# Performance work log

Measured on AMD Instinct MI355X. Metric: run time of the kernel, lower is better.

Reference implementation:

```python
import jax, jax.numpy as jnp
import numpy as np

SEQ, BATCH, IN_DIM, HID, LAYERS = 1024, 256, 64, 128, 2


def setup_inputs() -> dict:
    key = jax.random.key(0)
    ks = jax.random.split(key, 9)
    s = 1.0 / np.sqrt(HID)  # torch nn.RNN init: U(-1/sqrt(H), 1/sqrt(H))
    u = lambda k, shape: jax.random.uniform(k, shape, jnp.float32, -s, s)
    return {
        "x": jax.random.normal(ks[0], (SEQ, BATCH, IN_DIM), jnp.float32),
        "W_ih0": u(ks[1], (HID, IN_DIM)),
        "b_ih0": u(ks[2], (HID,)),
        "W_hh0": u(ks[3], (HID, HID)),
        "b_hh0": u(ks[4], (HID,)),
        "W_ih1": u(ks[5], (HID, HID)),
        "b_ih1": u(ks[6], (HID,)),
        "W_hh1": u(ks[7], (HID, HID)),
        "b_hh1": u(ks[8], (HID,)),
    }


def _rnn_layer(x, W_ih, b_ih, W_hh, b_hh):
    # x: (S, B, F). Precompute the input projection once (big GEMM),
    # keeping only the tiny h @ W_hh.T inside the sequential scan.
    xw = jnp.einsum('sbf,hf->sbh', x, W_ih) + b_ih + b_hh  # (S, B, H)
    h0 = jnp.zeros((x.shape[1], W_hh.shape[0]), x.dtype)

    def step(h, xw_t):
        h = jnp.tanh(xw_t + h @ W_hh.T)
        return h, h

    h_last, ys = jax.lax.scan(step, h0, xw)
    return ys, h_last  # (S, B, H), (B, H)


def reference(x, W_ih0, b_ih0, W_hh0, b_hh0, W_ih1, b_ih1, W_hh1, b_hh1):
    # 2-layer unidirectional Elman RNN with tanh (torch.nn.RNN, eval mode:
    # inter-layer dropout is identity at inference).
    y0, h0 = _rnn_layer(x, W_ih0, b_ih0, W_hh0, b_hh0)
    y1, h1 = _rnn_layer(y0, W_ih1, b_ih1, W_hh1, b_hh1)
    h_n = jnp.stack([h0, h1], axis=0)  # (num_layers, B, H)
    return y1, h_n
```

## Files before the change

kernel.cpp:

```cpp
#include <hip/hip_runtime.h>
#include <type_traits>


#define SEQ   1024
#define BATCH 256
#define FDIM  64
#define HID   128

typedef __attribute__((ext_vector_type(8))) _Float16 half8;
typedef __attribute__((ext_vector_type(4))) _Float16 half4v;
typedef __attribute__((ext_vector_type(2))) _Float16 half2v;
typedef __attribute__((ext_vector_type(4))) float    f32x4;

#define MFMA16(a, b, c) __builtin_amdgcn_mfma_f32_16x16x32_f16((a), (b), (c), 0, 0, 0)

__device__ __forceinline__ void lds_barrier() {
  asm volatile("s_waitcnt lgkmcnt(0)\n\ts_barrier" ::: "memory");
}

__device__ __forceinline__ float fast_tanh(float x) {
  float e = __builtin_amdgcn_exp2f(x * 2.8853900817779268f);
  return 1.0f - 2.0f * __builtin_amdgcn_rcpf(e + 1.0f);
}

__device__ __forceinline__ half8 cvt8(float4 a, float4 b) {
  half8 h;
  h[0] = (_Float16)a.x; h[1] = (_Float16)a.y; h[2] = (_Float16)a.z; h[3] = (_Float16)a.w;
  h[4] = (_Float16)b.x; h[5] = (_Float16)b.y; h[6] = (_Float16)b.z; h[7] = (_Float16)b.w;
  return h;
}

__device__ __forceinline__ half8 h8zero() {
  half8 v;
#pragma unroll
  for (int j = 0; j < 8; ++j) v[j] = (_Float16)0.0f;
  return v;
}

__device__ __forceinline__ half8 load_w_frag(const float* __restrict__ W,
                                             int row, int k0, int ld) {
  const float4* p = (const float4*)(W + row * ld + k0);
  float4 a = p[0], b = p[1];
  return cvt8(a, b);
}

__device__ __forceinline__ half8 load_w_perm(const float* __restrict__ W,
                                             int row, int q, int g4, int ld) {
  const float* p = W + row * ld + q * 4 + g4;
  half8 h;
#pragma unroll
  for (int j = 0; j < 8; ++j) h[j] = (_Float16)p[j * 16];
  return h;
}

__device__ __forceinline__ f32x4 seed_cvt(float4 v) {
  f32x4 r; r[0] = v.x; r[1] = v.y; r[2] = v.z; r[3] = v.w; return r;
}
__device__ __forceinline__ f32x4 seed_cvt(half4v v) {
  f32x4 r; r[0] = (float)v[0]; r[1] = (float)v[1]; r[2] = (float)v[2]; r[3] = (float)v[3];
  return r;
}

template<int XF32>
__global__ __launch_bounds__(256) void gemm_xw(
    const float* __restrict__ x, const float* __restrict__ Wih0,
    const float* __restrict__ bih0, const float* __restrict__ bhh0,
    void* __restrict__ xw)
{
  const int tid = threadIdx.x, w = tid >> 6, lane = tid & 63;
  const int r16 = lane & 15, g4 = lane >> 4;
  const size_t mbase = (size_t)blockIdx.x * 64 + w * 16;
  const size_t mblk  = (size_t)blockIdx.x * 4 + w;

  half8 Bw[8][2]; float bv[8];
#pragma unroll
  for (int n = 0; n < 8; ++n) {
    const int row = n * 16 + r16;
    Bw[n][0] = load_w_frag(Wih0, row, (g4 << 3), FDIM);
    Bw[n][1] = load_w_frag(Wih0, row, 32 + (g4 << 3), FDIM);
    bv[n] = bih0[row] + bhh0[row];
  }
  const float* xr = x + (mbase + r16) * FDIM + (g4 << 3);
  float4 x0 = *(const float4*)(xr),      x1 = *(const float4*)(xr + 4);
  float4 x2 = *(const float4*)(xr + 32), x3 = *(const float4*)(xr + 36);
  half8 A0 = cvt8(x0, x1), A1 = cvt8(x2, x3);

#pragma unroll
  for (int n = 0; n < 8; ++n) {
    f32x4 acc = {bv[n], bv[n], bv[n], bv[n]};
    acc = MFMA16(A0, Bw[n][0], acc);
    acc = MFMA16(A1, Bw[n][1], acc);
    const size_t idx = (mblk * 8 + n) * 64 + (g4 << 4) + r16;
    if constexpr (XF32) {
      float4 s; s.x = acc[0]; s.y = acc[1]; s.z = acc[2]; s.w = acc[3];
      ((float4*)xw)[idx] = s;
    } else {
      half4v s; s[0] = (_Float16)acc[0]; s[1] = (_Float16)acc[1];
      s[2] = (_Float16)acc[2]; s[3] = (_Float16)acc[3];
      ((half4v*)xw)[idx] = s;
    }
  }
}

template<int XF32>
__global__ __launch_bounds__(512, 1) void rnn_scan(
    const void* __restrict__ xwv,
    const float* __restrict__ Whh0,
    const float* __restrict__ Wih1, const float* __restrict__ bih1,
    const float* __restrict__ Whh1, const float* __restrict__ bhh1,
    float* __restrict__ out)
{
  using XT = typename std::conditional<XF32 != 0, float4, half4v>::type;
  __shared__ alignas(16) _Float16 hp[2][2][16][136];
  const int tid  = threadIdx.x;
  const int wgrp = tid >> 8;
  const int wv   = (tid >> 6) & 3;
  const int lane = tid & 63;
  const int r16  = lane & 15;
  const int g4   = lane >> 4;
  const int blk  = blockIdx.x;
  const int b0   = blk << 4;
  const bool isL0 = (wgrp == 0);

  half8 WA[2][4], WB[2][4];
  float bs[2];
#pragma unroll
  for (int n = 0; n < 2; ++n) {
    const int row = (wv << 5) + (n << 4) + r16;
    if (isL0) {
#pragma unroll
      for (int q = 0; q < 4; ++q) { WA[n][q] = load_w_perm(Whh0, row, q, g4, HID); WB[n][q] = h8zero(); }
      bs[n] = 0.f;
    } else {
#pragma unroll
      for (int q = 0; q < 4; ++q) {
        WB[n][q] = load_w_perm(Wih1, row, q, g4, HID);
        WA[n][q] = load_w_perm(Whh1, row, q, g4, HID);
      }
      bs[n] = bih1[row] + bhh1[row];
    }
  }

  half8 h0A[4], h1A[4];
#pragma unroll
  for (int q = 0; q < 4; ++q) { h0A[q] = h8zero(); h1A[q] = h8zero(); }

  const XT* xw = (const XT*)xwv;
  size_t xb0 = ((size_t)blk * 8 + (wv << 1)) * 64 + (g4 << 4) + r16;
  size_t xb1 = xb0 + 64;

  XT ring[4][2];
  if (isL0) {
    ring[0][0] = xw[xb0];            ring[0][1] = xw[xb1];
    ring[1][0] = xw[xb0 + 8192];     ring[1][1] = xw[xb1 + 8192];
    ring[2][0] = xw[xb0 + 16384];    ring[2][1] = xw[xb1 + 16384];
  }

  _Float16* wb = &hp[0][wgrp][g4 << 2][(r16 << 3) + (wv << 1)];
  const _Float16* rb = &hp[0][0][r16][g4 << 3];
  float* ybase = out + (size_t)(b0 + (g4 << 2)) * HID + (wv << 5) + r16;

  float hf[2][4];

#define RNN_BODY(k)                                                            \
  {                                                                            \
    const int t = t0 + (k);                                                    \
    _Float16* w = wb + (((k) & 1) * 4352);                                     \
    if (isL0) {                                                                \
      const int tp = (t + 3 < SEQ) ? (t + 3) : (SEQ - 1);                      \
      ring[((k) + 3) & 3][0] = xw[xb0 + (size_t)tp * 8192];                    \
      ring[((k) + 3) & 3][1] = xw[xb1 + (size_t)tp * 8192];                    \
      _Pragma("unroll")                                                        \
      for (int n = 0; n < 2; ++n) {                                            \
        f32x4 a0 = seed_cvt(ring[(k)][n]);                                     \
        f32x4 a1 = {0.f, 0.f, 0.f, 0.f};                                       \
        a0 = MFMA16(h0A[0], WA[n][0], a0);                                     \
        a1 = MFMA16(h0A[1], WA[n][1], a1);                                     \
        a0 = MFMA16(h0A[2], WA[n][2], a0);                                     \
        a1 = MFMA16(h0A[3], WA[n][3], a1);                                     \
        _Pragma("unroll")                                                      \
        for (int i = 0; i < 4; ++i) hf[n][i] = fast_tanh(a0[i] + a1[i]);       \
      }                                                                        \
      _Pragma("unroll")                                                        \
      for (int i = 0; i < 4; ++i) {                                            \
        half2v v; v[0] = (_Float16)hf[0][i]; v[1] = (_Float16)hf[1][i];        \
        *(half2v*)(w + i * 136) = v;                                           \
      }                                                                        \
    } else {                                                                   \
      _Pragma("unroll")                                                        \
      for (int n = 0; n < 2; ++n) {                                            \
        f32x4 a0 = {bs[n], bs[n], bs[n], bs[n]};                               \
        f32x4 a1 = {0.f, 0.f, 0.f, 0.f};                                       \
        f32x4 a2 = {0.f, 0.f, 0.f, 0.f};                                       \
        f32x4 a3 = {0.f, 0.f, 0.f, 0.f};                                       \
        a0 = MFMA16(h0A[0], WB[n][0], a0);                                     \
        a1 = MFMA16(h0A[1], WB[n][1], a1);                                     \
        a2 = MFMA16(h0A[2], WB[n][2], a2);                                     \
        a3 = MFMA16(h0A[3], WB[n][3], a3);                                     \
        a0 = MFMA16(h1A[0], WA[n][0], a0);                                     \
        a1 = MFMA16(h1A[1], WA[n][1], a1);                                     \
        a2 = MFMA16(h1A[2], WA[n][2], a2);                                     \
        a3 = MFMA16(h1A[3], WA[n][3], a3);                                     \
        _Pragma("unroll")                                                      \
        for (int i = 0; i < 4; ++i)                                            \
          hf[n][i] = fast_tanh((a0[i] + a1[i]) + (a2[i] + a3[i]));             \
      }                                                                        \
      if (t > 0) {                                                             \
        float* yo = ybase + (size_t)(t - 1) * (BATCH * HID);                   \
        _Pragma("unroll")                                                      \
        for (int n = 0; n < 2; ++n)                                            \
          _Pragma("unroll")                                                    \
          for (int i = 0; i < 4; ++i) yo[i * HID + n * 16] = hf[n][i];         \
      }                                                                        \
      _Pragma("unroll")                                                        \
      for (int i = 0; i < 4; ++i) {                                            \
        half2v v; v[0] = (_Float16)hf[0][i]; v[1] = (_Float16)hf[1][i];        \
        *(half2v*)(w + i * 136) = v;                                           \
      }                                                                        \
    }                                                                          \
    lds_barrier();                                                             \
    {                                                                          \
      const _Float16* r = rb + (((k) & 1) * 4352);                             \
      _Pragma("unroll")                                                        \
      for (int q = 0; q < 4; ++q) h0A[q] = *(const half8*)(r + q * 32);        \
      if (!isL0) {                                                             \
        _Pragma("unroll")                                                      \
        for (int q = 0; q < 4; ++q) h1A[q] = *(const half8*)(r + 2176 + q * 32);\
        if (t == 0) {                                                          \
          _Pragma("unroll")                                                    \
          for (int q = 0; q < 4; ++q) h1A[q] = h8zero();                       \
        }                                                                      \
      }                                                                        \
    }                                                                          \
  }

#pragma unroll 1
  for (int t0 = 0; t0 < SEQ; t0 += 4) {
    RNN_BODY(0)
    RNN_BODY(1)
    RNN_BODY(2)
    RNN_BODY(3)
  }
#undef RNN_BODY

  if (isL0) {
    float* hn0 = out + (size_t)SEQ * BATCH * HID +
                 (size_t)(b0 + (g4 << 2)) * HID + (wv << 5) + r16;
#pragma unroll
    for (int n = 0; n < 2; ++n)
#pragma unroll
      for (int i = 0; i < 4; ++i) hn0[i * HID + n * 16] = hf[n][i];
  } else {
    float h1l[2][4];
#pragma unroll
    for (int n = 0; n < 2; ++n) {
      f32x4 a0 = {bs[n], bs[n], bs[n], bs[n]};
      f32x4 a1 = {0.f, 0.f, 0.f, 0.f};
      f32x4 a2 = {0.f, 0.f, 0.f, 0.f};
      f32x4 a3 = {0.f, 0.f, 0.f, 0.f};
      a0 = MFMA16(h0A[0], WB[n][0], a0);
      a1 = MFMA16(h0A[1], WB[n][1], a1);
      a2 = MFMA16(h0A[2], WB[n][2], a2);
      a3 = MFMA16(h0A[3], WB[n][3], a3);
      a0 = MFMA16(h1A[0], WA[n][0], a0);
      a1 = MFMA16(h1A[1], WA[n][1], a1);
      a2 = MFMA16(h1A[2], WA[n][2], a2);
      a3 = MFMA16(h1A[3], WA[n][3], a3);
#pragma unroll
      for (int i = 0; i < 4; ++i)
        h1l[n][i] = fast_tanh((a0[i] + a1[i]) + (a2[i] + a3[i]));
    }
    float* yo = ybase + (size_t)(SEQ - 1) * (BATCH * HID);
    float* hn1 = out + (size_t)SEQ * BATCH * HID + (size_t)BATCH * HID +
                 (size_t)(b0 + (g4 << 2)) * HID + (wv << 5) + r16;
#pragma unroll
    for (int n = 0; n < 2; ++n)
#pragma unroll
      for (int i = 0; i < 4; ++i) {
        yo[i * HID + n * 16]  = h1l[n][i];
        hn1[i * HID + n * 16] = h1l[n][i];
      }
  }
}

extern "C" void kernel_launch(void* const* d_in, const int* in_sizes, int n_in,
                              void* d_out, int out_size, void* d_ws, size_t ws_size,
                              hipStream_t stream) {
  (void)in_sizes; (void)n_in; (void)out_size;
  const float* x    = (const float*)d_in[0];
  const float* Wih0 = (const float*)d_in[1];
  const float* bih0 = (const float*)d_in[2];
  const float* Whh0 = (const float*)d_in[3];
  const float* bhh0 = (const float*)d_in[4];
  const float* Wih1 = (const float*)d_in[5];
  const float* bih1 = (const float*)d_in[6];
  const float* Whh1 = (const float*)d_in[7];
  const float* bhh1 = (const float*)d_in[8];
  float* out = (float*)d_out;

  const size_t nelem = (size_t)SEQ * BATCH * HID;
  const int nblk_gemm = (SEQ * BATCH) / 64;

  if (ws_size >= nelem * 4) {
    gemm_xw<1><<<nblk_gemm, 256, 0, stream>>>(x, Wih0, bih0, bhh0, d_ws);
    rnn_scan<1><<<16, 512, 0, stream>>>(d_ws, Whh0, Wih1, bih1, Whh1, bhh1, out);
  } else {
    gemm_xw<0><<<nblk_gemm, 256, 0, stream>>>(x, Wih0, bih0, bhh0, d_ws);
    rnn_scan<0><<<16, 512, 0, stream>>>(d_ws, Whh0, Wih1, bih1, Whh1, bhh1, out);
  }
}
```

Measured before the change: 852.1 us.

## Repack LDS hidden-state layout, make GEMM blocks persistent, reorder L1 stores

The hidden-state LDS buffer is changed from a padded row-major layout to a packed fragment-ordered layout, so each lane reads its MFMA A fragments with contiguous 16-byte loads at lane*8 offsets. The W_hh permutation is changed to match the new k-ordering. The input-projection GEMM now runs 512 persistent blocks that each process 8 tiles and prefetch the next tile's x, which amortises the per-block weight loads. Layer 1 also writes h to LDS before its global y stores so the barrier is reached sooner. The risk is LDS bank conflicts in the new unpadded layout, and a permutation mismatch would produce incorrect results.

```diff
diff --git a/kernel.cpp b/kernel.cpp
--- a/kernel.cpp
+++ b/kernel.cpp
@@ -46,10 +46,10 @@
 
 __device__ __forceinline__ half8 load_w_perm(const float* __restrict__ W,
                                              int row, int q, int g4, int ld) {
-  const float* p = W + row * ld + q * 4 + g4;
+  const float* p = W + row * ld + q * 32 + g4 * 4;
   half8 h;
 #pragma unroll
-  for (int j = 0; j < 8; ++j) h[j] = (_Float16)p[j * 16];
+  for (int j = 0; j < 8; ++j) h[j] = (_Float16)p[(j & 1) * 16 + (j >> 1)];
   return h;
 }
 
@@ -69,8 +69,6 @@
 {
   const int tid = threadIdx.x, w = tid >> 6, lane = tid & 63;
   const int r16 = lane & 15, g4 = lane >> 4;
-  const size_t mbase = (size_t)blockIdx.x * 64 + w * 16;
-  const size_t mblk  = (size_t)blockIdx.x * 4 + w;
 
   half8 Bw[8][2]; float bv[8];
 #pragma unroll
@@ -80,25 +78,39 @@
     Bw[n][1] = load_w_frag(Wih0, row, 32 + (g4 << 3), FDIM);
     bv[n] = bih0[row] + bhh0[row];
   }
-  const float* xr = x + (mbase + r16) * FDIM + (g4 << 3);
-  float4 x0 = *(const float4*)(xr),      x1 = *(const float4*)(xr + 4);
-  float4 x2 = *(const float4*)(xr + 32), x3 = *(const float4*)(xr + 36);
-  half8 A0 = cvt8(x0, x1), A1 = cvt8(x2, x3);
-
-#pragma unroll
-  for (int n = 0; n < 8; ++n) {
-    f32x4 acc = {bv[n], bv[n], bv[n], bv[n]};
-    acc = MFMA16(A0, Bw[n][0], acc);
-    acc = MFMA16(A1, Bw[n][1], acc);
-    const size_t idx = (mblk * 8 + n) * 64 + (g4 << 4) + r16;
-    if constexpr (XF32) {
-      float4 s; s.x = acc[0]; s.y = acc[1]; s.z = acc[2]; s.w = acc[3];
-      ((float4*)xw)[idx] = s;
-    } else {
-      half4v s; s[0] = (_Float16)acc[0]; s[1] = (_Float16)acc[1];
-      s[2] = (_Float16)acc[2]; s[3] = (_Float16)acc[3];
-      ((half4v*)xw)[idx] = s;
+
+  int mt = blockIdx.x * 4 + w;
+  const float* xr = x + (size_t)(mt * 16 + r16) * FDIM + (g4 << 3);
+  float4 xp0 = *(const float4*)(xr),      xp1 = *(const float4*)(xr + 4);
+  float4 xp2 = *(const float4*)(xr + 32), xp3 = *(const float4*)(xr + 36);
+
+#pragma unroll
+  for (int rep = 0; rep < 8; ++rep) {
+    float4 n0, n1, n2, n3;
+    if (rep < 7) {
+      const float* xn = xr + (size_t)2048 * 16 * FDIM;
+      n0 = *(const float4*)(xn);      n1 = *(const float4*)(xn + 4);
+      n2 = *(const float4*)(xn + 32); n3 = *(const float4*)(xn + 36);
+      xr = xn;
     }
+    half8 A0 = cvt8(xp0, xp1), A1 = cvt8(xp2, xp3);
+#pragma unroll
+    for (int n = 0; n < 8; ++n) {
+      f32x4 acc = {bv[n], bv[n], bv[n], bv[n]};
+      acc = MFMA16(A0, Bw[n][0], acc);
+      acc = MFMA16(A1, Bw[n][1], acc);
+      const size_t idx = ((size_t)mt * 8 + n) * 64 + (g4 << 4) + r16;
+      if constexpr (XF32) {
+        float4 s; s.x = acc[0]; s.y = acc[1]; s.z = acc[2]; s.w = acc[3];
+        ((float4*)xw)[idx] = s;
+      } else {
+        half4v s; s[0] = (_Float16)acc[0]; s[1] = (_Float16)acc[1];
+        s[2] = (_Float16)acc[2]; s[3] = (_Float16)acc[3];
+        ((half4v*)xw)[idx] = s;
+      }
+    }
+    mt += 2048;
+    xp0 = n0; xp1 = n1; xp2 = n2; xp3 = n3;
   }
 }
 
@@ -111,7 +123,7 @@
     float* __restrict__ out)
 {
   using XT = typename std::conditional<XF32 != 0, float4, half4v>::type;
-  __shared__ alignas(16) _Float16 hp[2][2][16][136];
+  __shared__ alignas(16) _Float16 hp[2][2][2048];
   const int tid  = threadIdx.x;
   const int wgrp = tid >> 8;
   const int wv   = (tid >> 6) & 3;
@@ -156,8 +168,9 @@
     ring[2][0] = xw[xb0 + 16384];    ring[2][1] = xw[xb1 + 16384];
   }
 
-  _Float16* wb = &hp[0][wgrp][g4 << 2][(r16 << 3) + (wv << 1)];
-  const _Float16* rb = &hp[0][0][r16][g4 << 3];
+  _Float16* wb = &hp[0][wgrp][((wv << 2) + (r16 >> 2)) * 128 + (g4 << 5) + ((r16 & 3) << 1)];
+  const _Float16* rb = &hp[0][0][lane << 3];
+
   float* ybase = out + (size_t)(b0 + (g4 << 2)) * HID + (wv << 5) + r16;
 
   float hf[2][4];
@@ -165,7 +178,7 @@
 #define RNN_BODY(k)                                                            \
   {                                                                            \
     const int t = t0 + (k);                                                    \
-    _Float16* w = wb + (((k) & 1) * 4352);                                     \
+    _Float16* w = wb + (((k) & 1) * 4096);                                     \
     if (isL0) {                                                                \
       const int tp = (t + 3 < SEQ) ? (t + 3) : (SEQ - 1);                      \
       ring[((k) + 3) & 3][0] = xw[xb0 + (size_t)tp * 8192];                    \
@@ -184,7 +197,7 @@
       _Pragma("unroll")                                                        \
       for (int i = 0; i < 4; ++i) {                                            \
         half2v v; v[0] = (_Float16)hf[0][i]; v[1] = (_Float16)hf[1][i];        \
-        *(half2v*)(w + i * 136) = v;                                           \
+        *(half2v*)(w + i * 8) = v;                                             \
       }                                                                        \
     } else {                                                                   \
       _Pragma("unroll")                                                        \
@@ -205,6 +218,11 @@
         for (int i = 0; i < 4; ++i)                                            \
           hf[n][i] = fast_tanh((a0[i] + a1[i]) + (a2[i] + a3[i]));             \
       }                                                                        \
+      _Pragma("unroll")                                                        \
+      for (int i = 0; i < 4; ++i) {                                            \
+        half2v v; v[0] = (_Float16)hf[0][i]; v[1] = (_Float16)hf[1][i];        \
+        *(half2v*)(w + i * 8) = v;                                             \
+      }                                                                        \
       if (t > 0) {                                                             \
         float* yo = ybase + (size_t)(t - 1) * (BATCH * HID);                   \
         _Pragma("unroll")                                                      \
@@ -212,20 +230,15 @@
           _Pragma("unroll")                                                    \
           for (int i = 0; i < 4; ++i) yo[i * HID + n * 16] = hf[n][i];         \
       }                                                                        \
-      _Pragma("unroll")                                                        \
-      for (int i = 0; i < 4; ++i) {                                            \
-        half2v v; v[0] = (_Float16)hf[0][i]; v[1] = (_Float16)hf[1][i];        \
-        *(half2v*)(w + i * 136) = v;                                           \
-      }                                                                        \
     }                                                                          \
     lds_barrier();                                                             \
     {                                                                          \
-      const _Float16* r = rb + (((k) & 1) * 4352);                             \
-      _Pragma("unroll")                                                        \
-      for (int q = 0; q < 4; ++q) h0A[q] = *(const half8*)(r + q * 32);        \
+      const _Float16* r = rb + (((k) & 1) * 4096);                             \
+      _Pragma("unroll")                                                        \
+      for (int q = 0; q < 4; ++q) h0A[q] = *(const half8*)(r + q * 512);       \
       if (!isL0) {                                                             \
         _Pragma("unroll")                                                      \
-        for (int q = 0; q < 4; ++q) h1A[q] = *(const half8*)(r + 2176 + q * 32);\
+        for (int q = 0; q < 4; ++q) h1A[q] = *(const half8*)(r + 2048 + q * 512);\
         if (t == 0) {                                                          \
           _Pragma("unroll")                                                    \
           for (int q = 0; q < 4; ++q) h1A[q] = h8zero();                       \
@@ -299,13 +312,12 @@
   float* out = (float*)d_out;
 
   const size_t nelem = (size_t)SEQ * BATCH * HID;
-  const int nblk_gemm = (SEQ * BATCH) / 64;
 
   if (ws_size >= nelem * 4) {
-    gemm_xw<1><<<nblk_gemm, 256, 0, stream>>>(x, Wih0, bih0, bhh0, d_ws);
+    gemm_xw<1><<<512, 256, 0, stream>>>(x, Wih0, bih0, bhh0, d_ws);
     rnn_scan<1><<<16, 512, 0, stream>>>(d_ws, Whh0, Wih1, bih1, Whh1, bhh1, out);
   } else {
-    gemm_xw<0><<<nblk_gemm, 256, 0, stream>>>(x, Wih0, bih0, bhh0, d_ws);
+    gemm_xw<0><<<512, 256, 0, stream>>>(x, Wih0, bih0, bhh0, d_ws);
     rnn_scan<0><<<16, 512, 0, stream>>>(d_ws, Whh0, Wih1, bih1, Whh1, bhh1, out);
   }
 }
```

New measurement: 824.0 us. 1.03x faster.
